# Kernel optimization log

Hardware: AMD Instinct MI355X
Metric: run time of the kernel (lower is better)

The kernel has to match this reference:

```python
import jax, jax.numpy as jnp
import numpy as np

D = 128            # shared state dim for path/link/queue (required equal by scatter_nd)
T = 8              # message-passing iterations
NUM_POLICIES = 3
MAX_NUM_QUEUES = 3
READOUT = 256


def gru(x, h, W, U, b):
    # Keras GRUCell, reset_after=True. W:[F,3D], U:[D,3D], b:[2,3D]
    gi = x @ W + b[0]
    gh = h @ U + b[1]
    iz, ir, ih = jnp.split(gi, 3, axis=-1)
    hz, hr, hh = jnp.split(gh, 3, axis=-1)
    z = jax.nn.sigmoid(iz + hz)
    r = jax.nn.sigmoid(ir + hr)
    cand = jnp.tanh(ih + r * hh)
    return z * h + (1.0 - z) * cand


def masked_gru_rnn(x_seq, h0, W, U, b):
    # x_seq: [N, Tm, F]; Masking layer: skip timesteps whose features are all zero
    def step(h, xt):
        mask = jnp.any(xt != 0, axis=-1, keepdims=True)
        hn = gru(xt, h, W, U, b)
        return jnp.where(mask, hn, h), None
    h, _ = jax.lax.scan(step, h0, jnp.swapaxes(x_seq, 0, 1))
    return h


def setup_inputs() -> dict:
    rng = np.random.default_rng(0)
    N_PATHS, N_LINKS, L, QL = 20000, 4000, 8, 3
    N_QUEUES = N_LINKS * QL
    E = N_PATHS * L
    f32 = np.float32
    traffic = rng.random(N_PATHS, dtype=f32)
    packets = rng.random(N_PATHS, dtype=f32)
    capacity = rng.random(N_LINKS, dtype=f32)
    weight = rng.random(N_QUEUES, dtype=f32)
    policy = rng.integers(0, NUM_POLICIES, N_LINKS).astype(np.int32)
    priority = rng.integers(0, MAX_NUM_QUEUES, N_QUEUES).astype(np.int32)
    # each path traverses L links; hop positions are unique per path (scatter_nd well-defined)
    path_ids = np.repeat(np.arange(N_PATHS, dtype=np.int32), L)
    l_q_p = np.tile(np.arange(L, dtype=np.int32), N_PATHS)
    l_p_s = l_q_p.copy()
    link_to_path = rng.integers(0, N_LINKS, E).astype(np.int32)
    queue_to_path = (link_to_path * QL + rng.integers(0, QL, E)).astype(np.int32)
    path_to_queue = path_ids.copy()
    sequence_queues = queue_to_path.copy()
    queue_to_link = np.arange(N_QUEUES, dtype=np.int32)  # queue i belongs to link i//QL
    sequence_links = np.repeat(np.arange(N_LINKS, dtype=np.int32), QL)
    l_q_l = np.tile(np.arange(QL, dtype=np.int32), N_LINKS)

    def p(k, *shape):
        kk = jax.random.fold_in(jax.random.key(0), k)
        return jax.random.normal(kk, shape, jnp.float32) / np.sqrt(f32(shape[0]))

    params = dict(
        Wp=p(1, 2 * D, 3 * D), Up=p(2, D, 3 * D), bp=0.01 * p(3, 2, 3 * D),
        Wl=p(4, D, 3 * D), Ul=p(5, D, 3 * D), bl=0.01 * p(6, 2, 3 * D),
        Wq=p(7, D, 3 * D), Uq=p(8, D, 3 * D), bq=0.01 * p(9, 2, 3 * D),
        Wr1=p(10, D, READOUT), br1=jnp.zeros((READOUT,), jnp.float32),
        Wr2=p(11, READOUT, READOUT), br2=jnp.zeros((READOUT,), jnp.float32),
        Wr3=p(12, READOUT, 1), br3=jnp.zeros((1,), jnp.float32),
    )
    inp = dict(
        traffic=jnp.asarray(traffic), packets=jnp.asarray(packets),
        capacity=jnp.asarray(capacity), weight=jnp.asarray(weight),
        policy=jnp.asarray(policy), priority=jnp.asarray(priority),
        path_ids=jnp.asarray(path_ids), l_q_p=jnp.asarray(l_q_p), l_p_s=jnp.asarray(l_p_s),
        link_to_path=jnp.asarray(link_to_path), queue_to_path=jnp.asarray(queue_to_path),
        path_to_queue=jnp.asarray(path_to_queue), sequence_queues=jnp.asarray(sequence_queues),
        queue_to_link=jnp.asarray(queue_to_link), sequence_links=jnp.asarray(sequence_links),
        l_q_l=jnp.asarray(l_q_l), n_paths=N_PATHS, n_links=N_LINKS, n_queues=N_QUEUES,
    )
    inp.update(params)
    return inp


def reference(traffic, packets, capacity, weight, policy, priority, path_ids, l_q_p, l_p_s,
              link_to_path, queue_to_path, path_to_queue, sequence_queues, queue_to_link,
              sequence_links, l_q_l, n_paths, n_links, n_queues,
              Wp, Up, bp, Wl, Ul, bl, Wq, Uq, bq, Wr1, br1, Wr2, br2, Wr3, br3):
    path_state = jnp.concatenate([traffic[:, None], packets[:, None],
                                  jnp.zeros((n_paths, D - 2), jnp.float32)], axis=1)
    link_state = jnp.concatenate([capacity[:, None],
                                  jax.nn.one_hot(policy, NUM_POLICIES, dtype=jnp.float32),
                                  jnp.zeros((n_links, D - NUM_POLICIES - 1), jnp.float32)], axis=1)
    queue_state = jnp.concatenate([jax.nn.one_hot(priority, MAX_NUM_QUEUES, dtype=jnp.float32),
                                   weight[:, None],
                                   jnp.zeros((n_queues, D - MAX_NUM_QUEUES - 1), jnp.float32)], axis=1)
    max_p = int(np.asarray(l_q_p).max()) + 1
    max_l = int(np.asarray(l_q_l).max()) + 1
    for _ in range(T):
        # paths: gather link+queue states, scatter into padded sequences, run masked GRU
        qg = queue_state[queue_to_path]                       # [E, D]
        lg = link_state[link_to_path]                         # [E, D]
        qi = jnp.zeros((n_paths, max_p, D), jnp.float32).at[path_ids, l_q_p].add(qg)
        li = jnp.zeros((n_paths, max_p, D), jnp.float32).at[path_ids, l_p_s].add(lg)
        path_state = masked_gru_rnn(jnp.concatenate([qi, li], axis=2), path_state, Wp, Up, bp)
        # queues: sum path states per queue, single GRU cell step
        path_sum = jax.ops.segment_sum(path_state[path_to_queue], sequence_queues,
                                       num_segments=n_queues)
        queue_state = gru(path_sum, queue_state, Wq, Uq, bq)
        # links: gather queue states into padded sequences, masked GRU
        qi2 = jnp.zeros((n_links, max_l, D), jnp.float32).at[sequence_links, l_q_l].add(
            queue_state[queue_to_link])
        link_state = masked_gru_rnn(qi2, link_state, Wl, Ul, bl)
    h = jax.nn.relu(path_state @ Wr1 + br1)
    h = jax.nn.relu(h @ Wr2 + br2)
    return h @ Wr3 + br3
```

## Files before the change

### kernel.cpp

```cpp
#include <hip/hip_runtime.h>
#include <hip/hip_bf16.h>
#include <hip/hip_fp16.h>
#include <math.h>

#define NP 20000
#define NL 4000
#define NQ 12000
#define NE 160000
#define DD 128
#define N3 384
#define TT 8
#define FR 512

typedef __attribute__((ext_vector_type(8))) short bf16x8;
typedef __attribute__((ext_vector_type(4))) float f32x4;

__device__ float g_path [NP * DD];
__device__ float g_link [NL * DD];
__device__ float g_queue[NQ * DD];
__device__ unsigned short g_qgi_h[NQ * N3];
__device__ unsigned short g_lgi_h[NL * N3];
__device__ float g_psum [NQ * DD];
__device__ int   g_peq  [NE];
__device__ int   g_pel  [NE];
__device__ int   g_counts[NQ];
__device__ int   g_off  [NQ + 1];
__device__ int   g_cur  [NQ];
__device__ int   g_col  [NE];
__device__ int   g_nzq  [NQ];
__device__ int   g_nzl  [NL];
__device__ unsigned short g_upb_hi[24*4*FR], g_upb_lo[24*4*FR];
__device__ unsigned short g_wpb_hi[2*24*4*FR], g_wpb_lo[2*24*4*FR];
__device__ unsigned short g_wlb_hi[24*4*FR], g_wlb_lo[24*4*FR];
__device__ unsigned short g_wuq_hi[24*8*FR], g_wuq_lo[24*8*FR];
__device__ unsigned short g_ulb_hi[24*4*FR], g_ulb_lo[24*4*FR];
__device__ unsigned short g_w1b_hi[16*4*FR], g_w1b_lo[16*4*FR];
__device__ unsigned short g_w2b_hi[16*8*FR], g_w2b_lo[16*8*FR];

__device__ __forceinline__ float fsig(float x)  { return 1.0f / (1.0f + __expf(-x)); }
__device__ __forceinline__ float ftanh(float x) { return 2.0f / (1.0f + __expf(-2.0f * x)) - 1.0f; }

__device__ __forceinline__ void split_bf(float v, unsigned short& hi, unsigned short& lo) {
    unsigned u = __float_as_uint(v);
    hi = (unsigned short)(u >> 16);
    float lof = v - __uint_as_float(u & 0xFFFF0000u);
    lo = (unsigned short)(__float_as_uint(lof) >> 16);
}
__device__ __forceinline__ unsigned short f2h(float v) {
    __half h = __float2half_rn(v);
    return *reinterpret_cast<unsigned short*>(&h);
}
__device__ __forceinline__ float h2f(unsigned short u) {
    __half h = *reinterpret_cast<__half*>(&u);
    return __half2float(h);
}

__global__ void k_init_maps() {
    int i = blockIdx.x * 256 + threadIdx.x;
    if (i < NE) { g_peq[i] = -1; g_pel[i] = -1; }
    if (i < NQ) { g_counts[i] = 0; }
}

__global__ void k_fill_maps(const int* __restrict__ path_ids, const int* __restrict__ l_q_p,
                            const int* __restrict__ l_p_s, const int* __restrict__ queue_to_path,
                            const int* __restrict__ link_to_path, const int* __restrict__ sequence_queues) {
    int i = blockIdx.x * 256 + threadIdx.x;
    if (i < NE) {
        int p = path_ids[i];
        g_peq[p * 8 + l_q_p[i]] = queue_to_path[i];
        g_pel[p * 8 + l_p_s[i]] = link_to_path[i];
        atomicAdd(&g_counts[sequence_queues[i]], 1);
    }
}

__global__ __launch_bounds__(1024) void k_scan() {
    __shared__ int part[1024];
    int tid = threadIdx.x;
    int base = tid * 12;
    int local[12];
    int s = 0;
#pragma unroll
    for (int j = 0; j < 12; j++) {
        int idx = base + j;
        int v = (idx < NQ) ? g_counts[idx] : 0;
        local[j] = s; s += v;
    }
    part[tid] = s;
    __syncthreads();
    for (int off = 1; off < 1024; off <<= 1) {
        int v = (tid >= off) ? part[tid - off] : 0;
        __syncthreads();
        part[tid] += v;
        __syncthreads();
    }
    int pre = (tid > 0) ? part[tid - 1] : 0;
#pragma unroll
    for (int j = 0; j < 12; j++) {
        int idx = base + j;
        if (idx < NQ) { g_off[idx] = pre + local[j]; g_cur[idx] = pre + local[j]; }
    }
    if (tid == 1023) g_off[NQ] = part[1023];
}

__global__ void k_fill_csr(const int* __restrict__ sequence_queues, const int* __restrict__ path_to_queue) {
    int i = blockIdx.x * 256 + threadIdx.x;
    if (i < NE) {
        int q = sequence_queues[i];
        int pos = atomicAdd(&g_cur[q], 1);
        g_col[pos] = path_to_queue[i];
    }
}

__global__ void k_init_states(const float* __restrict__ traffic, const float* __restrict__ packets,
                              const float* __restrict__ capacity, const int* __restrict__ policy,
                              const float* __restrict__ weight, const int* __restrict__ priority) {
    int idx = blockIdx.x * 256 + threadIdx.x;
    if (idx < NP * DD) {
        int p = idx >> 7, d = idx & 127;
        g_path[idx] = (d == 0) ? traffic[p] : (d == 1) ? packets[p] : 0.0f;
    }
    if (idx < NL * DD) {
        int l = idx >> 7, d = idx & 127;
        float v = 0.0f;
        if (d == 0) v = capacity[l];
        else if (d >= 1 && d <= 3) v = (policy[l] == d - 1) ? 1.0f : 0.0f;
        g_link[idx] = v;
    }
    if (idx < NQ * DD) {
        int q = idx >> 7, d = idx & 127;
        float v = 0.0f;
        if (d < 3) v = (priority[q] == d) ? 1.0f : 0.0f;
        else if (d == 3) v = weight[q];
        g_queue[idx] = v;
    }
}

__global__ void k_pack(int mode, const float* __restrict__ W, int ldn) {
    unsigned short *dhi, *dlo;
    int nt_cnt, kc_cnt, kc_total, kc_base;
    if (mode == 0)      { dhi=g_upb_hi; dlo=g_upb_lo; nt_cnt=24; kc_cnt=4; kc_total=4; kc_base=0; }
    else if (mode == 1) { dhi=g_wpb_hi; dlo=g_wpb_lo; nt_cnt=24; kc_cnt=4; kc_total=4; kc_base=0; }
    else if (mode == 2) { dhi=g_wpb_hi+24*4*FR; dlo=g_wpb_lo+24*4*FR; nt_cnt=24; kc_cnt=4; kc_total=4; kc_base=0; }
    else if (mode == 3) { dhi=g_wlb_hi; dlo=g_wlb_lo; nt_cnt=24; kc_cnt=4; kc_total=4; kc_base=0; }
    else if (mode == 4) { dhi=g_wuq_hi; dlo=g_wuq_lo; nt_cnt=24; kc_cnt=4; kc_total=8; kc_base=0; }
    else if (mode == 5) { dhi=g_wuq_hi; dlo=g_wuq_lo; nt_cnt=24; kc_cnt=4; kc_total=8; kc_base=4; }
    else if (mode == 6) { dhi=g_ulb_hi; dlo=g_ulb_lo; nt_cnt=24; kc_cnt=4; kc_total=4; kc_base=0; }
    else if (mode == 7) { dhi=g_w1b_hi; dlo=g_w1b_lo; nt_cnt=16; kc_cnt=4; kc_total=4; kc_base=0; }
    else                { dhi=g_w2b_hi; dlo=g_w2b_lo; nt_cnt=16; kc_cnt=8; kc_total=8; kc_base=0; }
    int tot = nt_cnt * kc_cnt * FR;
    int idx = blockIdx.x * 256 + threadIdx.x;
    if (idx >= tot) return;
    int j = idx & 7, lane = (idx >> 3) & 63;
    int kc = (idx >> 9) % kc_cnt, nt = idx / (kc_cnt * FR);
    int k = kc * 32 + (lane >> 4) * 8 + j;
    int col = nt * 16 + (lane & 15);
    float v = W[(size_t)k * ldn + col];
    unsigned short hi, lo;
    split_bf(v, hi, lo);
    size_t o = ((size_t)(nt * kc_total + kc_base + kc)) * FR + (size_t)lane * 8 + j;
    dhi[o] = hi; dlo[o] = lo;
}

__global__ void k_nz(int mode) {
    const float* st = mode ? g_link : g_queue;
    int n = mode ? NL : NQ;
    int* outf = mode ? g_nzl : g_nzq;
    int w = threadIdx.x >> 6, lane = threadIdx.x & 63;
    int row = blockIdx.x * 4 + w;
    if (row < n) {
        const float* r = st + (size_t)row * DD;
        bool nz = (r[lane] != 0.0f) || (r[lane + 64] != 0.0f);
        unsigned long long b = __ballot(nz);
        if (lane == 0) outf[row] = (b != 0ULL) ? 1 : 0;
    }
}

__global__ __launch_bounds__(256) void k_gemm_mfma(int mode, const float* __restrict__ bias) {
    const float* A; unsigned short* C; const unsigned short *Bh, *Bl;
    int r0; bool useB;
    if (mode == 2) {
        A = g_queue; C = g_qgi_h; Bh = g_wlb_hi; Bl = g_wlb_lo;
        r0 = blockIdx.x * 16; useB = true;
    } else {
        if (blockIdx.x < NQ / 16) {
            A = g_queue; C = g_qgi_h; Bh = g_wpb_hi; Bl = g_wpb_lo;
            r0 = blockIdx.x * 16; useB = true;
        } else {
            A = g_link; C = g_lgi_h; Bh = g_wpb_hi + 24*4*FR; Bl = g_wpb_lo + 24*4*FR;
            r0 = (blockIdx.x - NQ / 16) * 16; useB = false;
        }
    }
    __shared__ unsigned short as_hi[16][136], as_lo[16][136];
    const int tid = threadIdx.x, w = tid >> 6, l = tid & 63;
    for (int idx = tid; idx < 16 * DD; idx += 256) {
        unsigned short hi, lo;
        split_bf(A[(size_t)r0 * DD + idx], hi, lo);
        as_hi[idx >> 7][idx & 127] = hi; as_lo[idx >> 7][idx & 127] = lo;
    }
    __syncthreads();
    f32x4 acc[6];
#pragma unroll
    for (int n = 0; n < 6; n++) acc[n] = (f32x4){0.f, 0.f, 0.f, 0.f};
#pragma unroll
    for (int kc = 0; kc < 4; kc++) {
        int kk = kc * 32 + (l >> 4) * 8;
        bf16x8 ah = *reinterpret_cast<const bf16x8*>(&as_hi[l & 15][kk]);
        bf16x8 al = *reinterpret_cast<const bf16x8*>(&as_lo[l & 15][kk]);
#pragma unroll
        for (int n = 0; n < 6; n++) {
            int nt = 6 * w + n;
            size_t boff = ((size_t)(nt * 4 + kc)) * FR + (size_t)l * 8;
            bf16x8 bhv = *reinterpret_cast<const bf16x8*>(&Bh[boff]);
            bf16x8 blv = *reinterpret_cast<const bf16x8*>(&Bl[boff]);
            acc[n] = __builtin_amdgcn_mfma_f32_16x16x32_bf16(ah, bhv, acc[n], 0, 0, 0);
            acc[n] = __builtin_amdgcn_mfma_f32_16x16x32_bf16(al, bhv, acc[n], 0, 0, 0);
            acc[n] = __builtin_amdgcn_mfma_f32_16x16x32_bf16(ah, blv, acc[n], 0, 0, 0);
        }
    }
    const int rbase = (l >> 4) * 4;
#pragma unroll
    for (int n = 0; n < 6; n++) {
        int col = (6 * w + n) * 16 + (l & 15);
        float bv = useB ? bias[col] : 0.f;
#pragma unroll
        for (int i = 0; i < 4; i++)
            C[(size_t)(r0 + rbase + i) * N3 + col] = f2h(acc[n][i] + bv);
    }
}

__global__ __launch_bounds__(512, 2) void k_path(const float* __restrict__ bp) {
    __shared__ unsigned short hs_hi[2][16][136];
    __shared__ unsigned short hs_lo[2][16][136];
    __shared__ int qqA[8][16], llA[8][16], mAsh[8][16];
    const int tid = threadIdx.x;
    const int w = tid >> 6, l = tid & 63;
    const int r0 = blockIdx.x * 16;
    if (tid < 128) {
        int r = tid >> 3, t = tid & 7;
        int e = (r0 + r) * 8 + t;
        int qq = g_peq[e], ll = g_pel[e];
        qqA[t][r] = qq; llA[t][r] = ll;
        mAsh[t][r] = (g_nzq[qq] | g_nzl[ll]);
    }
    const int c0 = 16 * w + (l & 15);
    const int rbase = (l >> 4) * 4;
    bf16x8 Bh[12], Bl[12];
#pragma unroll
    for (int kc = 0; kc < 4; kc++) {
#pragma unroll
        for (int g = 0; g < 3; g++) {
            int nt = g * 8 + w;
            size_t boff = ((size_t)(nt * 4 + kc) * 64 + l) * 8;
            Bh[kc * 3 + g] = *reinterpret_cast<const bf16x8*>(&g_upb_hi[boff]);
            Bl[kc * 3 + g] = *reinterpret_cast<const bf16x8*>(&g_upb_lo[boff]);
        }
    }
    float h0[4];
#pragma unroll
    for (int i = 0; i < 4; i++)
        h0[i] = g_path[(size_t)(r0 + rbase + i) * DD + c0];
#pragma unroll
    for (int i = 0; i < 4; i++) {
        unsigned short hi, lo;
        split_bf(h0[i], hi, lo);
        hs_hi[0][rbase + i][c0] = hi; hs_lo[0][rbase + i][c0] = lo;
    }
    __syncthreads();
    const float bz = bp[N3 + c0], br = bp[N3 + 128 + c0], bh = bp[N3 + 256 + c0];

    unsigned short pq[2][4][3], pl[2][4][3];
#pragma unroll
    for (int i = 0; i < 4; i++) {
        int q = qqA[0][rbase + i], lk = llA[0][rbase + i];
        const unsigned short* qp = g_qgi_h + (size_t)q * N3 + c0;
        const unsigned short* lp = g_lgi_h + (size_t)lk * N3 + c0;
        pq[0][i][0] = qp[0]; pq[0][i][1] = qp[128]; pq[0][i][2] = qp[256];
        pl[0][i][0] = lp[0]; pl[0][i][1] = lp[128]; pl[0][i][2] = lp[256];
    }

#pragma unroll
    for (int t = 0; t < TT; t++) {
        const int cur = t & 1, nxt = cur ^ 1;
        if (t + 1 < TT) {
#pragma unroll
            for (int i = 0; i < 4; i++) {
                int q = qqA[t + 1][rbase + i], lk = llA[t + 1][rbase + i];
                const unsigned short* qp = g_qgi_h + (size_t)q * N3 + c0;
                const unsigned short* lp = g_lgi_h + (size_t)lk * N3 + c0;
                pq[nxt][i][0] = qp[0]; pq[nxt][i][1] = qp[128]; pq[nxt][i][2] = qp[256];
                pl[nxt][i][0] = lp[0]; pl[nxt][i][1] = lp[128]; pl[nxt][i][2] = lp[256];
            }
        }
        int msk[4];
#pragma unroll
        for (int i = 0; i < 4; i++) msk[i] = mAsh[t][rbase + i];

        bf16x8 ah[4], al[4];
#pragma unroll
        for (int kc = 0; kc < 4; kc++) {
            ah[kc] = *reinterpret_cast<const bf16x8*>(&hs_hi[cur][l & 15][kc * 32 + (l >> 4) * 8]);
            al[kc] = *reinterpret_cast<const bf16x8*>(&hs_lo[cur][l & 15][kc * 32 + (l >> 4) * 8]);
        }
        f32x4 acc[3];
#pragma unroll
        for (int g = 0; g < 3; g++) acc[g] = (f32x4){0.f, 0.f, 0.f, 0.f};
#pragma unroll
        for (int kc = 0; kc < 4; kc++) {
#pragma unroll
            for (int g = 0; g < 3; g++) {
                bf16x8 bhv = Bh[kc * 3 + g];
                bf16x8 blv = Bl[kc * 3 + g];
                acc[g] = __builtin_amdgcn_mfma_f32_16x16x32_bf16(ah[kc], bhv, acc[g], 0, 0, 0);
                acc[g] = __builtin_amdgcn_mfma_f32_16x16x32_bf16(al[kc], bhv, acc[g], 0, 0, 0);
                acc[g] = __builtin_amdgcn_mfma_f32_16x16x32_bf16(ah[kc], blv, acc[g], 0, 0, 0);
            }
        }
#pragma unroll
        for (int i = 0; i < 4; i++) {
            float gz = h2f(pq[cur][i][0]) + h2f(pl[cur][i][0]);
            float gr = h2f(pq[cur][i][1]) + h2f(pl[cur][i][1]);
            float gh = h2f(pq[cur][i][2]) + h2f(pl[cur][i][2]);
            float zin = acc[0][i] + gz + bz;
            float rin = acc[1][i] + gr + br;
            float zv = fsig(zin);
            float rv = fsig(rin);
            float cand = ftanh(gh + rv * (acc[2][i] + bh));
            float hn = zv * h0[i] + (1.0f - zv) * cand;
            h0[i] = msk[i] ? hn : h0[i];
        }
#pragma unroll
        for (int i = 0; i < 4; i++) {
            unsigned short hi, lo;
            split_bf(h0[i], hi, lo);
            hs_hi[nxt][rbase + i][c0] = hi; hs_lo[nxt][rbase + i][c0] = lo;
        }
        __syncthreads();
    }
#pragma unroll
    for (int i = 0; i < 4; i++)
        g_path[(size_t)(r0 + rbase + i) * DD + c0] = h0[i];
}

__global__ void k_qsum() {
    int w = threadIdx.x >> 6, lane = threadIdx.x & 63;
    int q = blockIdx.x * 4 + w;
    if (q >= NQ) return;
    int s = g_off[q], e = g_off[q + 1];
    float a0 = 0.f, a1 = 0.f;
    for (int i = s; i < e; i++) {
        const float* p = g_path + (size_t)g_col[i] * DD;
        a0 += p[lane]; a1 += p[lane + 64];
    }
    g_psum[(size_t)q * DD + lane] = a0;
    g_psum[(size_t)q * DD + lane + 64] = a1;
}

__global__ __launch_bounds__(256) void k_queue_mfma(const float* __restrict__ bq) {
    __shared__ unsigned short xs_hi[16][136], xs_lo[16][136];
    __shared__ unsigned short hs_hi[16][136], hs_lo[16][136];
    __shared__ int nzf[16];
    const int tid = threadIdx.x, w = tid >> 6, l = tid & 63;
    const int r0 = blockIdx.x * 16;
    if (tid < 16) nzf[tid] = 0;
    for (int idx = tid; idx < 16 * DD; idx += 256) {
        unsigned short hi, lo;
        split_bf(g_psum[(size_t)r0 * DD + idx], hi, lo);
        xs_hi[idx >> 7][idx & 127] = hi; xs_lo[idx >> 7][idx & 127] = lo;
        split_bf(g_queue[(size_t)r0 * DD + idx], hi, lo);
        hs_hi[idx >> 7][idx & 127] = hi; hs_lo[idx >> 7][idx & 127] = lo;
    }
    __syncthreads();
    f32x4 aZ[2], aR[2], aIH[2], aHH[2];
#pragma unroll
    for (int tau = 0; tau < 2; tau++) {
        aZ[tau] = (f32x4){0.f,0.f,0.f,0.f}; aR[tau] = (f32x4){0.f,0.f,0.f,0.f};
        aIH[tau] = (f32x4){0.f,0.f,0.f,0.f}; aHH[tau] = (f32x4){0.f,0.f,0.f,0.f};
    }
#pragma unroll
    for (int kc = 0; kc < 8; kc++) {
        int kk = (kc & 3) * 32 + (l >> 4) * 8;
        bf16x8 ah, al;
        if (kc < 4) {
            ah = *reinterpret_cast<const bf16x8*>(&xs_hi[l & 15][kk]);
            al = *reinterpret_cast<const bf16x8*>(&xs_lo[l & 15][kk]);
        } else {
            ah = *reinterpret_cast<const bf16x8*>(&hs_hi[l & 15][kk]);
            al = *reinterpret_cast<const bf16x8*>(&hs_lo[l & 15][kk]);
        }
#pragma unroll
        for (int g = 0; g < 3; g++) {
#pragma unroll
            for (int tau = 0; tau < 2; tau++) {
                int nt = g * 8 + 2 * w + tau;
                size_t boff = ((size_t)(nt * 8 + kc)) * FR + (size_t)l * 8;
                bf16x8 bhv = *reinterpret_cast<const bf16x8*>(&g_wuq_hi[boff]);
                bf16x8 blv = *reinterpret_cast<const bf16x8*>(&g_wuq_lo[boff]);
                f32x4 a = (g == 0) ? aZ[tau] : (g == 1) ? aR[tau] : (kc < 4 ? aIH[tau] : aHH[tau]);
                a = __builtin_amdgcn_mfma_f32_16x16x32_bf16(ah, bhv, a, 0, 0, 0);
                a = __builtin_amdgcn_mfma_f32_16x16x32_bf16(al, bhv, a, 0, 0, 0);
                a = __builtin_amdgcn_mfma_f32_16x16x32_bf16(ah, blv, a, 0, 0, 0);
                if (g == 0) aZ[tau] = a; else if (g == 1) aR[tau] = a;
                else { if (kc < 4) aIH[tau] = a; else aHH[tau] = a; }
            }
        }
    }
    const int rbase = (l >> 4) * 4;
#pragma unroll
    for (int tau = 0; tau < 2; tau++) {
        int c = 32 * w + (l & 15) + (tau ? 16 : 0);
        float bz0 = bq[c],       bz1 = bq[N3 + c];
        float br0 = bq[128 + c], br1 = bq[N3 + 128 + c];
        float bh0 = bq[256 + c], bh1 = bq[N3 + 256 + c];
#pragma unroll
        for (int i = 0; i < 4; i++) {
            size_t row = (size_t)(r0 + rbase + i);
            float hold = g_queue[row * DD + c];
            float z = fsig(aZ[tau][i] + bz0 + bz1);
            float r = fsig(aR[tau][i] + br0 + br1);
            float cand = ftanh(aIH[tau][i] + bh0 + r * (aHH[tau][i] + bh1));
            float hn = z * hold + (1.0f - z) * cand;
            g_queue[row * DD + c] = hn;
            if (hn != 0.0f) nzf[rbase + i] = 1;
        }
    }
    __syncthreads();
    if (tid < 16) g_nzq[r0 + tid] = nzf[tid];
}

__global__ __launch_bounds__(256) void k_link_mfma(const float* __restrict__ bl) {
    __shared__ unsigned short hs_hi[16][136], hs_lo[16][136];
    __shared__ int mA[3][16], nzf[16];
    const int tid = threadIdx.x, w = tid >> 6, l = tid & 63;
    const int r0 = blockIdx.x * 16;
    if (tid < 16) nzf[tid] = 0;
    if (tid < 48) {
        int r = tid / 3, j = tid % 3;
        mA[j][r] = g_nzq[3 * (r0 + r) + j];
    }
    const int c0 = 32 * w + (l & 15), c1 = c0 + 16;
    const int rbase = (l >> 4) * 4;
    float h0[4], h1[4];
#pragma unroll
    for (int i = 0; i < 4; i++) {
        h0[i] = g_link[(size_t)(r0 + rbase + i) * DD + c0];
        h1[i] = g_link[(size_t)(r0 + rbase + i) * DD + c1];
    }
#pragma unroll
    for (int i = 0; i < 4; i++) {
        unsigned short hi, lo;
        split_bf(h0[i], hi, lo); hs_hi[rbase + i][c0] = hi; hs_lo[rbase + i][c0] = lo;
        split_bf(h1[i], hi, lo); hs_hi[rbase + i][c1] = hi; hs_lo[rbase + i][c1] = lo;
    }
    __syncthreads();
    float bz[2], br[2], bh[2];
    bz[0] = bl[N3 + c0]; bz[1] = bl[N3 + c1];
    br[0] = bl[N3 + 128 + c0]; br[1] = bl[N3 + 128 + c1];
    bh[0] = bl[N3 + 256 + c0]; bh[1] = bl[N3 + 256 + c1];

    for (int t = 0; t < 3; t++) {
        int msk[4];
#pragma unroll
        for (int i = 0; i < 4; i++) msk[i] = mA[t][rbase + i];
        float gq[2][4][3];
#pragma unroll
        for (int tau = 0; tau < 2; tau++) {
            int cc = tau ? c1 : c0;
#pragma unroll
            for (int i = 0; i < 4; i++) {
                int q = 3 * (r0 + rbase + i) + t;
                const unsigned short* qp = g_qgi_h + (size_t)q * N3 + cc;
                gq[tau][i][0] = h2f(qp[0]); gq[tau][i][1] = h2f(qp[128]); gq[tau][i][2] = h2f(qp[256]);
            }
        }
        bf16x8 ah[4], al[4];
#pragma unroll
        for (int kc = 0; kc < 4; kc++) {
            ah[kc] = *reinterpret_cast<const bf16x8*>(&hs_hi[l & 15][kc * 32 + (l >> 4) * 8]);
            al[kc] = *reinterpret_cast<const bf16x8*>(&hs_lo[l & 15][kc * 32 + (l >> 4) * 8]);
        }
        f32x4 acc[3][2];
#pragma unroll
        for (int g = 0; g < 3; g++)
#pragma unroll
            for (int tau = 0; tau < 2; tau++) acc[g][tau] = (f32x4){0.f, 0.f, 0.f, 0.f};
#pragma unroll
        for (int kc = 0; kc < 4; kc++) {
#pragma unroll
            for (int g = 0; g < 3; g++) {
#pragma unroll
                for (int tau = 0; tau < 2; tau++) {
                    int nt = g * 8 + 2 * w + tau;
                    size_t boff = ((size_t)(nt * 4 + kc)) * FR + (size_t)l * 8;
                    bf16x8 bhv = *reinterpret_cast<const bf16x8*>(&g_ulb_hi[boff]);
                    bf16x8 blv = *reinterpret_cast<const bf16x8*>(&g_ulb_lo[boff]);
                    acc[g][tau] = __builtin_amdgcn_mfma_f32_16x16x32_bf16(ah[kc], bhv, acc[g][tau], 0, 0, 0);
                    acc[g][tau] = __builtin_amdgcn_mfma_f32_16x16x32_bf16(al[kc], bhv, acc[g][tau], 0, 0, 0);
                    acc[g][tau] = __builtin_amdgcn_mfma_f32_16x16x32_bf16(ah[kc], blv, acc[g][tau], 0, 0, 0);
                }
            }
        }
        __syncthreads();
#pragma unroll
        for (int tau = 0; tau < 2; tau++) {
#pragma unroll
            for (int i = 0; i < 4; i++) {
                float zin = acc[0][tau][i] + gq[tau][i][0] + bz[tau];
                float rin = acc[1][tau][i] + gq[tau][i][1] + br[tau];
                float hold = tau ? h1[i] : h0[i];
                float zv = fsig(zin);
                float rv = fsig(rin);
                float cand = ftanh(gq[tau][i][2] + rv * (acc[2][tau][i] + bh[tau]));
                float hn = zv * hold + (1.0f - zv) * cand;
                float hout = msk[i] ? hn : hold;
                if (tau) h1[i] = hout; else h0[i] = hout;
            }
        }
#pragma unroll
        for (int i = 0; i < 4; i++) {
            unsigned short hi, lo;
            split_bf(h0[i], hi, lo); hs_hi[rbase + i][c0] = hi; hs_lo[rbase + i][c0] = lo;
            split_bf(h1[i], hi, lo); hs_hi[rbase + i][c1] = hi; hs_lo[rbase + i][c1] = lo;
        }
        __syncthreads();
    }
#pragma unroll
    for (int i = 0; i < 4; i++) {
        g_link[(size_t)(r0 + rbase + i) * DD + c0] = h0[i];
        g_link[(size_t)(r0 + rbase + i) * DD + c1] = h1[i];
        if (h0[i] != 0.0f || h1[i] != 0.0f) nzf[rbase + i] = 1;
    }
    __syncthreads();
    if (tid < 16) g_nzl[r0 + tid] = nzf[tid];
}

__global__ __launch_bounds__(256) void k_readout_mfma(const float* __restrict__ b1,
                                                      const float* __restrict__ b2,
                                                      const float* __restrict__ W3,
                                                      const float* __restrict__ b3,
                                                      float* __restrict__ out) {
    __shared__ unsigned short s1_hi[16][136], s1_lo[16][136];
    __shared__ unsigned short r1_hi[16][264], r1_lo[16][264];
    __shared__ float r2f[16][256];
    const int tid = threadIdx.x, w = tid >> 6, l = tid & 63;
    const int r0 = blockIdx.x * 16;
    for (int idx = tid; idx < 16 * DD; idx += 256) {
        unsigned short hi, lo;
        split_bf(g_path[(size_t)r0 * DD + idx], hi, lo);
        s1_hi[idx >> 7][idx & 127] = hi; s1_lo[idx >> 7][idx & 127] = lo;
    }
    __syncthreads();
    const int rbase = (l >> 4) * 4;
    {
        f32x4 acc[4];
#pragma unroll
        for (int n = 0; n < 4; n++) acc[n] = (f32x4){0.f, 0.f, 0.f, 0.f};
#pragma unroll
        for (int kc = 0; kc < 4; kc++) {
            int kk = kc * 32 + (l >> 4) * 8;
            bf16x8 ah = *reinterpret_cast<const bf16x8*>(&s1_hi[l & 15][kk]);
            bf16x8 al = *reinterpret_cast<const bf16x8*>(&s1_lo[l & 15][kk]);
#pragma unroll
            for (int n = 0; n < 4; n++) {
                int nt = 4 * w + n;
                size_t boff = ((size_t)(nt * 4 + kc)) * FR + (size_t)l * 8;
                bf16x8 bhv = *reinterpret_cast<const bf16x8*>(&g_w1b_hi[boff]);
                bf16x8 blv = *reinterpret_cast<const bf16x8*>(&g_w1b_lo[boff]);
                acc[n] = __builtin_amdgcn_mfma_f32_16x16x32_bf16(ah, bhv, acc[n], 0, 0, 0);
                acc[n] = __builtin_amdgcn_mfma_f32_16x16x32_bf16(al, bhv, acc[n], 0, 0, 0);
                acc[n] = __builtin_amdgcn_mfma_f32_16x16x32_bf16(ah, blv, acc[n], 0, 0, 0);
            }
        }
#pragma unroll
        for (int n = 0; n < 4; n++) {
            int col = (4 * w + n) * 16 + (l & 15);
#pragma unroll
            for (int i = 0; i < 4; i++) {
                float v = fmaxf(acc[n][i] + b1[col], 0.f);
                unsigned short hi, lo;
                split_bf(v, hi, lo);
                r1_hi[rbase + i][col] = hi; r1_lo[rbase + i][col] = lo;
            }
        }
    }
    __syncthreads();
    {
        f32x4 acc[4];
#pragma unroll
        for (int n = 0; n < 4; n++) acc[n] = (f32x4){0.f, 0.f, 0.f, 0.f};
#pragma unroll
        for (int kc = 0; kc < 8; kc++) {
            int kk = kc * 32 + (l >> 4) * 8;
            bf16x8 ah = *reinterpret_cast<const bf16x8*>(&r1_hi[l & 15][kk]);
            bf16x8 al = *reinterpret_cast<const bf16x8*>(&r1_lo[l & 15][kk]);
#pragma unroll
            for (int n = 0; n < 4; n++) {
                int nt = 4 * w + n;
                size_t boff = ((size_t)(nt * 8 + kc)) * FR + (size_t)l * 8;
                bf16x8 bhv = *reinterpret_cast<const bf16x8*>(&g_w2b_hi[boff]);
                bf16x8 blv = *reinterpret_cast<const bf16x8*>(&g_w2b_lo[boff]);
                acc[n] = __builtin_amdgcn_mfma_f32_16x16x32_bf16(ah, bhv, acc[n], 0, 0, 0);
                acc[n] = __builtin_amdgcn_mfma_f32_16x16x32_bf16(al, bhv, acc[n], 0, 0, 0);
                acc[n] = __builtin_amdgcn_mfma_f32_16x16x32_bf16(ah, blv, acc[n], 0, 0, 0);
            }
        }
#pragma unroll
        for (int n = 0; n < 4; n++) {
            int col = (4 * w + n) * 16 + (l & 15);
#pragma unroll
            for (int i = 0; i < 4; i++)
                r2f[rbase + i][col] = fmaxf(acc[n][i] + b2[col], 0.f);
        }
    }
    __syncthreads();
    {
        float w3a = W3[l], w3b = W3[l + 64], w3c = W3[l + 128], w3d = W3[l + 192];
#pragma unroll
        for (int rr = 0; rr < 4; rr++) {
            int row = w * 4 + rr;
            float s = r2f[row][l] * w3a + r2f[row][l + 64] * w3b +
                      r2f[row][l + 128] * w3c + r2f[row][l + 192] * w3d;
            for (int off = 32; off > 0; off >>= 1) s += __shfl_down(s, off);
            if (l == 0) out[r0 + row] = s + b3[0];
        }
    }
}

extern "C" void kernel_launch(void* const* d_in, const int* in_sizes, int n_in,
                              void* d_out, int out_size, void* d_ws, size_t ws_size,
                              hipStream_t stream) {
    const float* traffic  = (const float*)d_in[0];
    const float* packets  = (const float*)d_in[1];
    const float* capacity = (const float*)d_in[2];
    const float* weight   = (const float*)d_in[3];
    const int* policy     = (const int*)d_in[4];
    const int* priority   = (const int*)d_in[5];
    const int* path_ids   = (const int*)d_in[6];
    const int* l_q_p      = (const int*)d_in[7];
    const int* l_p_s      = (const int*)d_in[8];
    const int* link_to_path    = (const int*)d_in[9];
    const int* queue_to_path   = (const int*)d_in[10];
    const int* path_to_queue   = (const int*)d_in[11];
    const int* sequence_queues = (const int*)d_in[12];
    const float* Wp  = (const float*)d_in[19];
    const float* Up  = (const float*)d_in[20];
    const float* bp  = (const float*)d_in[21];
    const float* Wl  = (const float*)d_in[22];
    const float* Ul  = (const float*)d_in[23];
    const float* bl  = (const float*)d_in[24];
    const float* Wq  = (const float*)d_in[25];
    const float* Uq  = (const float*)d_in[26];
    const float* bq  = (const float*)d_in[27];
    const float* Wr1 = (const float*)d_in[28];
    const float* br1 = (const float*)d_in[29];
    const float* Wr2 = (const float*)d_in[30];
    const float* br2 = (const float*)d_in[31];
    const float* Wr3 = (const float*)d_in[32];
    const float* br3 = (const float*)d_in[33];
    float* out = (float*)d_out;

    k_init_maps<<<(NE + 255) / 256, 256, 0, stream>>>();
    k_fill_maps<<<(NE + 255) / 256, 256, 0, stream>>>(path_ids, l_q_p, l_p_s, queue_to_path,
                                                      link_to_path, sequence_queues);
    k_scan<<<1, 1024, 0, stream>>>();
    k_fill_csr<<<(NE + 255) / 256, 256, 0, stream>>>(sequence_queues, path_to_queue);
    k_init_states<<<(NP * DD + 255) / 256, 256, 0, stream>>>(traffic, packets, capacity,
                                                             policy, weight, priority);
    k_pack<<<192, 256, 0, stream>>>(0, Up, N3);
    k_pack<<<192, 256, 0, stream>>>(1, Wp, N3);
    k_pack<<<192, 256, 0, stream>>>(2, Wp + 128 * N3, N3);
    k_pack<<<192, 256, 0, stream>>>(3, Wl, N3);
    k_pack<<<192, 256, 0, stream>>>(4, Wq, N3);
    k_pack<<<192, 256, 0, stream>>>(5, Uq, N3);
    k_pack<<<192, 256, 0, stream>>>(6, Ul, N3);
    k_pack<<<128, 256, 0, stream>>>(7, Wr1, 256);
    k_pack<<<256, 256, 0, stream>>>(8, Wr2, 256);
    k_nz<<<NQ / 4, 256, 0, stream>>>(0);
    k_nz<<<NL / 4, 256, 0, stream>>>(1);

    for (int it = 0; it < TT; ++it) {
        k_gemm_mfma<<<NQ / 16 + NL / 16, 256, 0, stream>>>(3, bp);
        k_path<<<NP / 16, 512, 0, stream>>>(bp);
        k_qsum<<<NQ / 4, 256, 0, stream>>>();
        k_queue_mfma<<<NQ / 16, 256, 0, stream>>>(bq);
        k_gemm_mfma<<<NQ / 16, 256, 0, stream>>>(2, bl);
        k_link_mfma<<<NL / 16, 256, 0, stream>>>(bl);
    }

    k_readout_mfma<<<NP / 16, 256, 0, stream>>>(br1, br2, Wr3, br3, out);
}
```

Before: 1.597 ms.

## Fuse input-projection GEMMs into queue and link update kernels

The per-iteration projection GEMMs (queue state times Wl and Wp, link state times Wp) are folded into the epilogues of the queue and link GRU kernels, reusing the freshly computed state already held in shared memory. A second buffer for the queue-to-link projection is added so the path-projection of queues can be written in the same kernel. This removes two kernel launches per iteration and the re-read and re-split of the queue and link states, at the cost of heavier queue and link kernels with extra registers and MFMA work per block.

```diff
diff --git a/kernel.cpp b/kernel.cpp
--- a/kernel.cpp
+++ b/kernel.cpp
@@ -18,8 +18,9 @@
 __device__ float g_path [NP * DD];
 __device__ float g_link [NL * DD];
 __device__ float g_queue[NQ * DD];
-__device__ unsigned short g_qgi_h[NQ * N3];
-__device__ unsigned short g_lgi_h[NL * N3];
+__device__ unsigned short g_qgi_h [NQ * N3];
+__device__ unsigned short g_qgi2_h[NQ * N3];
+__device__ unsigned short g_lgi_h [NL * N3];
 __device__ float g_psum [NQ * DD];
 __device__ int   g_peq  [NE];
 __device__ int   g_pel  [NE];
@@ -175,20 +176,15 @@
     }
 }
 
-__global__ __launch_bounds__(256) void k_gemm_mfma(int mode, const float* __restrict__ bias) {
+__global__ __launch_bounds__(256) void k_gemm_mfma(const float* __restrict__ bias) {
     const float* A; unsigned short* C; const unsigned short *Bh, *Bl;
     int r0; bool useB;
-    if (mode == 2) {
-        A = g_queue; C = g_qgi_h; Bh = g_wlb_hi; Bl = g_wlb_lo;
+    if (blockIdx.x < NQ / 16) {
+        A = g_queue; C = g_qgi_h; Bh = g_wpb_hi; Bl = g_wpb_lo;
         r0 = blockIdx.x * 16; useB = true;
     } else {
-        if (blockIdx.x < NQ / 16) {
-            A = g_queue; C = g_qgi_h; Bh = g_wpb_hi; Bl = g_wpb_lo;
-            r0 = blockIdx.x * 16; useB = true;
-        } else {
-            A = g_link; C = g_lgi_h; Bh = g_wpb_hi + 24*4*FR; Bl = g_wpb_lo + 24*4*FR;
-            r0 = (blockIdx.x - NQ / 16) * 16; useB = false;
-        }
+        A = g_link; C = g_lgi_h; Bh = g_wpb_hi + 24*4*FR; Bl = g_wpb_lo + 24*4*FR;
+        r0 = (blockIdx.x - NQ / 16) * 16; useB = false;
     }
     __shared__ unsigned short as_hi[16][136], as_lo[16][136];
     const int tid = threadIdx.x, w = tid >> 6, l = tid & 63;
@@ -355,7 +351,9 @@
     g_psum[(size_t)q * DD + lane + 64] = a1;
 }
 
-__global__ __launch_bounds__(256) void k_queue_mfma(const float* __restrict__ bq) {
+__global__ __launch_bounds__(256) void k_queue_mfma(const float* __restrict__ bq,
+                                                    const float* __restrict__ bl,
+                                                    const float* __restrict__ bp) {
     __shared__ unsigned short xs_hi[16][136], xs_lo[16][136];
     __shared__ unsigned short hs_hi[16][136], hs_lo[16][136];
     __shared__ int nzf[16];
@@ -405,6 +403,7 @@
         }
     }
     const int rbase = (l >> 4) * 4;
+    float hnv[2][4];
 #pragma unroll
     for (int tau = 0; tau < 2; tau++) {
         int c = 32 * w + (l & 15) + (tau ? 16 : 0);
@@ -420,11 +419,82 @@
             float cand = ftanh(aIH[tau][i] + bh0 + r * (aHH[tau][i] + bh1));
             float hn = z * hold + (1.0f - z) * cand;
             g_queue[row * DD + c] = hn;
+            hnv[tau][i] = hn;
             if (hn != 0.0f) nzf[rbase + i] = 1;
         }
     }
     __syncthreads();
     if (tid < 16) g_nzq[r0 + tid] = nzf[tid];
+#pragma unroll
+    for (int tau = 0; tau < 2; tau++) {
+        int c = 32 * w + (l & 15) + (tau ? 16 : 0);
+#pragma unroll
+        for (int i = 0; i < 4; i++) {
+            unsigned short hi, lo;
+            split_bf(hnv[tau][i], hi, lo);
+            hs_hi[rbase + i][c] = hi; hs_lo[rbase + i][c] = lo;
+        }
+    }
+    __syncthreads();
+    bf16x8 ah[4], al[4];
+#pragma unroll
+    for (int kc = 0; kc < 4; kc++) {
+        int kk = kc * 32 + (l >> 4) * 8;
+        ah[kc] = *reinterpret_cast<const bf16x8*>(&hs_hi[l & 15][kk]);
+        al[kc] = *reinterpret_cast<const bf16x8*>(&hs_lo[l & 15][kk]);
+    }
+    {
+        f32x4 acc[6];
+#pragma unroll
+        for (int n = 0; n < 6; n++) acc[n] = (f32x4){0.f, 0.f, 0.f, 0.f};
+#pragma unroll
+        for (int kc = 0; kc < 4; kc++) {
+#pragma unroll
+            for (int n = 0; n < 6; n++) {
+                int nt = 6 * w + n;
+                size_t boff = ((size_t)(nt * 4 + kc)) * FR + (size_t)l * 8;
+                bf16x8 bhv = *reinterpret_cast<const bf16x8*>(&g_wlb_hi[boff]);
+                bf16x8 blv = *reinterpret_cast<const bf16x8*>(&g_wlb_lo[boff]);
+                acc[n] = __builtin_amdgcn_mfma_f32_16x16x32_bf16(ah[kc], bhv, acc[n], 0, 0, 0);
+                acc[n] = __builtin_amdgcn_mfma_f32_16x16x32_bf16(al[kc], bhv, acc[n], 0, 0, 0);
+                acc[n] = __builtin_amdgcn_mfma_f32_16x16x32_bf16(ah[kc], blv, acc[n], 0, 0, 0);
+            }
+        }
+#pragma unroll
+        for (int n = 0; n < 6; n++) {
+            int col = (6 * w + n) * 16 + (l & 15);
+            float bv = bl[col];
+#pragma unroll
+            for (int i = 0; i < 4; i++)
+                g_qgi2_h[(size_t)(r0 + rbase + i) * N3 + col] = f2h(acc[n][i] + bv);
+        }
+    }
+    {
+        f32x4 acc[6];
+#pragma unroll
+        for (int n = 0; n < 6; n++) acc[n] = (f32x4){0.f, 0.f, 0.f, 0.f};
+#pragma unroll
+        for (int kc = 0; kc < 4; kc++) {
+#pragma unroll
+            for (int n = 0; n < 6; n++) {
+                int nt = 6 * w + n;
+                size_t boff = ((size_t)(nt * 4 + kc)) * FR + (size_t)l * 8;
+                bf16x8 bhv = *reinterpret_cast<const bf16x8*>(&g_wpb_hi[boff]);
+                bf16x8 blv = *reinterpret_cast<const bf16x8*>(&g_wpb_lo[boff]);
+                acc[n] = __builtin_amdgcn_mfma_f32_16x16x32_bf16(ah[kc], bhv, acc[n], 0, 0, 0);
+                acc[n] = __builtin_amdgcn_mfma_f32_16x16x32_bf16(al[kc], bhv, acc[n], 0, 0, 0);
+                acc[n] = __builtin_amdgcn_mfma_f32_16x16x32_bf16(ah[kc], blv, acc[n], 0, 0, 0);
+            }
+        }
+#pragma unroll
+        for (int n = 0; n < 6; n++) {
+            int col = (6 * w + n) * 16 + (l & 15);
+            float bv = bp[col];
+#pragma unroll
+            for (int i = 0; i < 4; i++)
+                g_qgi_h[(size_t)(r0 + rbase + i) * N3 + col] = f2h(acc[n][i] + bv);
+        }
+    }
 }
 
 __global__ __launch_bounds__(256) void k_link_mfma(const float* __restrict__ bl) {
@@ -468,7 +538,7 @@
 #pragma unroll
             for (int i = 0; i < 4; i++) {
                 int q = 3 * (r0 + rbase + i) + t;
-                const unsigned short* qp = g_qgi_h + (size_t)q * N3 + cc;
+                const unsigned short* qp = g_qgi2_h + (size_t)q * N3 + cc;
                 gq[tau][i][0] = h2f(qp[0]); gq[tau][i][1] = h2f(qp[128]); gq[tau][i][2] = h2f(qp[256]);
             }
         }
@@ -531,6 +601,38 @@
     }
     __syncthreads();
     if (tid < 16) g_nzl[r0 + tid] = nzf[tid];
+    {
+        bf16x8 ah[4], al[4];
+#pragma unroll
+        for (int kc = 0; kc < 4; kc++) {
+            int kk = kc * 32 + (l >> 4) * 8;
+            ah[kc] = *reinterpret_cast<const bf16x8*>(&hs_hi[l & 15][kk]);
+            al[kc] = *reinterpret_cast<const bf16x8*>(&hs_lo[l & 15][kk]);
+        }
+        f32x4 acc[6];
+#pragma unroll
+        for (int n = 0; n < 6; n++) acc[n] = (f32x4){0.f, 0.f, 0.f, 0.f};
+#pragma unroll
+        for (int kc = 0; kc < 4; kc++) {
+#pragma unroll
+            for (int n = 0; n < 6; n++) {
+                int nt = 6 * w + n;
+                size_t boff = ((size_t)(nt * 4 + kc)) * FR + (size_t)l * 8;
+                bf16x8 bhv = *reinterpret_cast<const bf16x8*>(&g_wpb_hi[24*4*FR + boff]);
+                bf16x8 blv = *reinterpret_cast<const bf16x8*>(&g_wpb_lo[24*4*FR + boff]);
+                acc[n] = __builtin_amdgcn_mfma_f32_16x16x32_bf16(ah[kc], bhv, acc[n], 0, 0, 0);
+                acc[n] = __builtin_amdgcn_mfma_f32_16x16x32_bf16(al[kc], bhv, acc[n], 0, 0, 0);
+                acc[n] = __builtin_amdgcn_mfma_f32_16x16x32_bf16(ah[kc], blv, acc[n], 0, 0, 0);
+            }
+        }
+#pragma unroll
+        for (int n = 0; n < 6; n++) {
+            int col = (6 * w + n) * 16 + (l & 15);
+#pragma unroll
+            for (int i = 0; i < 4; i++)
+                g_lgi_h[(size_t)(r0 + rbase + i) * N3 + col] = f2h(acc[n][i]);
+        }
+    }
 }
 
 __global__ __launch_bounds__(256) void k_readout_mfma(const float* __restrict__ b1,
@@ -676,13 +778,12 @@
     k_pack<<<256, 256, 0, stream>>>(8, Wr2, 256);
     k_nz<<<NQ / 4, 256, 0, stream>>>(0);
     k_nz<<<NL / 4, 256, 0, stream>>>(1);
+    k_gemm_mfma<<<NQ / 16 + NL / 16, 256, 0, stream>>>(bp);
 
     for (int it = 0; it < TT; ++it) {
-        k_gemm_mfma<<<NQ / 16 + NL / 16, 256, 0, stream>>>(3, bp);
         k_path<<<NP / 16, 512, 0, stream>>>(bp);
         k_qsum<<<NQ / 4, 256, 0, stream>>>();
-        k_queue_mfma<<<NQ / 16, 256, 0, stream>>>(bq);
-        k_gemm_mfma<<<NQ / 16, 256, 0, stream>>>(2, bl);
+        k_queue_mfma<<<NQ / 16, 256, 0, stream>>>(bq, bl, bp);
         k_link_mfma<<<NL / 16, 256, 0, stream>>>(bl);
     }
 
```

Measured after the change: 1.557 ms. -2.5%, faster.
